# Optimization experiments

Measured on AMD Instinct MI355X. Metric: run time of the kernel, lower is better.

The kernel has to match this reference:

```python
import jax, jax.numpy as jnp
import numpy as np

EPS = 1e-06


def _create_circular_masks(h, w):
    # Faithful to the torch code: y spans width, x spans height -> mask shape (w, h).
    # Only used with square feature maps (h == w), matching the module's implicit assumption.
    cen_w, cen_h = w // 2, h // 2
    y = np.arange(-cen_w, w - cen_w).reshape(-1, 1)
    x = np.arange(-cen_h, h - cen_h).reshape(1, -1)
    y2, x2 = y * y, x * x
    r2 = x2 + y2
    masks = [r2 <= 0]
    max_r = int(np.sqrt(r2.max())) + 1
    quadrants = [(1, 1), (-1, 1), (1, -1), (-1, -1)]  # (sign_x, sign_y)
    for radius in range(1, max_r):
        lo, hi = (radius - 1) ** 2, radius ** 2
        for sx, sy in quadrants:
            quad = (sx * x >= 0) & (sy * y >= 0)
            masks.append((r2 > lo) & (r2 <= hi) & quad)  # ring mask
            masks.append((r2 <= hi) & quad)              # circle mask
    return np.stack(masks).astype(np.float32)  # [M, w, h] == [M, h, w] for square maps


def _l2_normalize(v):
    # v: [B, C]; torch norms over dim=1 with eps added to the norm
    return v / (jnp.linalg.norm(v, axis=1, keepdims=True) + EPS)


def setup_inputs() -> dict:
    key = jax.random.key(0)
    x = jax.random.normal(key, (32, 1024, 28, 28), dtype=jnp.float32)
    return {"x": x}


def reference(x) -> jnp.ndarray:
    B, C, H, W = x.shape
    masks = jnp.asarray(_create_circular_masks(H, W))  # [M, H, W] static constant
    # Global descriptor: max-pool over full map, then channel-wise L2 normalize.
    v = _l2_normalize(jnp.max(x, axis=(2, 3)))  # [B, C]
    # Accumulate masked-max descriptors; scan over the (fixed) mask set keeps
    # peak memory at one masked feature map instead of M of them.
    def step(acc, mask):
        vt = jnp.max(x * mask, axis=(2, 3))  # masked max-pool (zeros included, as in torch)
        return acc + _l2_normalize(vt), None
    v, _ = jax.lax.scan(step, v, masks)
    return v[:, :, None, None]  # [B, C, 1, 1] to match F.max_pool2d output shape
```

## Files before the change

kernel.cpp:

```cpp
#include <hip/hip_runtime.h>
#include <math.h>

#define B_DIM 32
#define C_DIM 1024
#define HW 28
#define MAP (HW * HW)
#define NMASK 153
#define NTERM 154
#define NBIN 77
#define DUMMY_BIN 77
#define MAXS 28

struct Sched {
    unsigned short tab[MAXS][64];
    unsigned char  split[64];
    unsigned char  binA[64];
    unsigned char  binB[64];
    bool ok;
};

constexpr Sched build_sched() {
    Sched S{};
    short px[NBIN][40] = {};
    int   n[NBIN] = {};
    for (int i = 0; i < 28; ++i)
        for (int j = 0; j < 28; ++j) {
            int dy = i - 14, dx = j - 14, r2 = dx * dx + dy * dy;
            int p = i * 28 + j;
            if (r2 == 0) { px[0][n[0]++] = (short)p; continue; }
            if (r2 > 361) continue;
            int r = 0; while (r * r < r2) ++r;
            const int sx[4] = {1, -1, 1, -1}, sy[4] = {1, 1, -1, -1};
            for (int q = 0; q < 4; ++q)
                if (sx[q] * dx >= 0 && sy[q] * dy >= 0) {
                    int b = 1 + q * 19 + (r - 1);
                    px[b][n[b]++] = (short)p;
                }
        }
    int ord[NBIN] = {};
    for (int k = 0; k < NBIN; ++k) ord[k] = k;
    for (int a = 0; a < NBIN; ++a) {
        int best = a;
        for (int b2 = a + 1; b2 < NBIN; ++b2)
            if (n[ord[b2]] > n[ord[best]]) best = b2;
        int t = ord[a]; ord[a] = ord[best]; ord[best] = t;
    }
    S.ok = true;
    for (int k = 0; k < NBIN; ++k) if (n[k] < 1 || n[k] > 40) S.ok = false;
    for (int l = 0; l < 64; ++l) {
        int bA = ord[l];
        int bB = (l >= 51) ? ord[64 + (63 - l)] : -1;
        int s = 0;
        for (int t = 0; t < n[bA] && s < MAXS; ++t) S.tab[s++][l] = (unsigned short)px[bA][t];
        S.split[l] = (unsigned char)s;
        S.binA[l]  = (unsigned char)bA;
        int fillpix;
        if (bB >= 0) {
            for (int t = 0; t < n[bB]; ++t) {
                if (s >= MAXS) { S.ok = false; break; }
                S.tab[s++][l] = (unsigned short)px[bB][t];
            }
            S.binB[l] = (unsigned char)bB;
            fillpix = px[bB][0];
        } else {
            S.binB[l] = DUMMY_BIN;
            fillpix = 406;
        }
        if (n[bA] > MAXS) S.ok = false;
        for (; s < MAXS; ++s) S.tab[s][l] = (unsigned short)fillpix;
    }
    return S;
}

static_assert(build_sched().ok, "schedule overflow / empty bin");
__constant__ Sched d_sched = build_sched();

__global__ __launch_bounds__(256) void cac_stage1(const float* __restrict__ x,
                                                  float* __restrict__ vt) {
    __shared__ __align__(16) float smap[4][MAP];
    __shared__ float sbin[4][NBIN + 1];
    __shared__ float spref[4][4][20];

    const int wave = threadIdx.x >> 6;
    const int lane = threadIdx.x & 63;
    const int pair = blockIdx.x * 4 + wave;

    const float4* xp4 = (const float4*)(x + (size_t)pair * MAP);
    float4* sm4 = (float4*)smap[wave];
    float gmax = -INFINITY;
    #pragma unroll
    for (int it = 0; it < 3; ++it) {
        float4 v = xp4[it * 64 + lane];
        sm4[it * 64 + lane] = v;
        gmax = fmaxf(fmaxf(gmax, fmaxf(v.x, v.y)), fmaxf(v.z, v.w));
    }
    if (lane < 4) {
        float4 v = xp4[192 + lane];
        sm4[192 + lane] = v;
        gmax = fmaxf(fmaxf(gmax, fmaxf(v.x, v.y)), fmaxf(v.z, v.w));
    }
    __syncthreads();

    const int split = d_sched.split[lane];
    float m1 = 0.0f, m2 = 0.0f;
    #pragma unroll
    for (int s = 0; s < MAXS; ++s) {
        float v = smap[wave][d_sched.tab[s][lane]];
        if (s < split) m1 = fmaxf(m1, v);
        else           m2 = fmaxf(m2, v);
    }
    sbin[wave][d_sched.binA[lane]] = m1;
    sbin[wave][d_sched.binB[lane]] = m2;

    #pragma unroll
    for (int off = 32; off; off >>= 1)
        gmax = fmaxf(gmax, __shfl_xor(gmax, off, 64));
    __syncthreads();

    if (lane < 4) {
        float run = sbin[wave][0];
        #pragma unroll
        for (int r = 1; r < 20; ++r) {
            run = fmaxf(run, sbin[wave][1 + lane * 19 + (r - 1)]);
            spref[wave][lane][r] = run;
        }
    }
    __syncthreads();

    const int b = pair >> 10;
    const int c = pair & (C_DIM - 1);
    float* outp = vt + (size_t)b * NTERM * C_DIM + c;
    for (int k = lane; k < NTERM; k += 64) {
        float val;
        if (k == 0) {
            val = sbin[wave][0];
        } else if (k == NMASK) {
            val = gmax;
        } else {
            int t = k - 1;
            int r = (t >> 3) + 1;
            int q = (t >> 1) & 3;
            val = (t & 1) ? spref[wave][q][r]
                          : sbin[wave][1 + q * 19 + (r - 1)];
        }
        outp[(size_t)k * C_DIM] = val;
    }
}

__global__ __launch_bounds__(256) void cac_stage2(const float* __restrict__ vt,
                                                  float* __restrict__ invn) {
    const int bm = blockIdx.x;
    const float4* p = (const float4*)(vt + (size_t)bm * C_DIM);
    float4 v = p[threadIdx.x];
    float s = v.x * v.x + v.y * v.y + v.z * v.z + v.w * v.w;
    __shared__ float red[4];
    #pragma unroll
    for (int off = 32; off; off >>= 1) s += __shfl_xor(s, off, 64);
    if ((threadIdx.x & 63) == 0) red[threadIdx.x >> 6] = s;
    __syncthreads();
    if (threadIdx.x == 0) {
        float t = red[0] + red[1] + red[2] + red[3];
        invn[bm] = 1.0f / (sqrtf(t) + 1e-6f);
    }
}

__global__ __launch_bounds__(256) void cac_stage3(const float* __restrict__ vt,
                                                  const float* __restrict__ invn,
                                                  float* __restrict__ out) {
    const int tid = blockIdx.x * 256 + threadIdx.x;
    const int b = tid >> 10;
    const int c = tid & (C_DIM - 1);
    const float* p  = vt + (size_t)b * NTERM * C_DIM + c;
    const float* nv = invn + b * NTERM;
    float acc0 = 0.0f, acc1 = 0.0f;
    #pragma unroll 7
    for (int m = 0; m < 154; m += 2) {
        acc0 += p[(size_t)m * C_DIM] * nv[m];
        acc1 += p[(size_t)(m + 1) * C_DIM] * nv[m + 1];
    }
    out[tid] = acc0 + acc1;
}

extern "C" void kernel_launch(void* const* d_in, const int* in_sizes, int n_in,
                              void* d_out, int out_size, void* d_ws, size_t ws_size,
                              hipStream_t stream) {
    const float* x = (const float*)d_in[0];
    float* out = (float*)d_out;

    float* vt   = (float*)d_ws;
    float* invn = vt + (size_t)B_DIM * NTERM * C_DIM;

    cac_stage1<<<(B_DIM * C_DIM) / 4, 256, 0, stream>>>(x, vt);
    cac_stage2<<<B_DIM * NTERM, 256, 0, stream>>>(vt, invn);
    cac_stage3<<<(B_DIM * C_DIM) / 256, 256, 0, stream>>>(vt, invn, out);
}
```

Baseline: 177.0 us.

## Store descriptors per pair contiguously, fuse norm partials, bank-balance LDS gathers

Stage 1 now writes each (b,c) pair's 160-term row contiguously instead of a strided [B,M,C] layout. It also emits per-block partial sums of squares, so stage 2 only reduces 256 partials per term rather than rereading the whole descriptor tensor. The gather schedule is split into separate 28-slot and 6-slot loops with byte offsets chosen at compile time to spread LDS bank load, which removes the per-iteration split branch. Stage 3 does float4 dot products over contiguous rows against shared inverse norms. In exchange the workspace grows with padding and a partials buffer, and stage B has only 32 blocks.

New measurement: 167.7 us. 5.3% less time.

```diff
diff --git a/kernel.cpp b/kernel.cpp
--- a/kernel.cpp
+++ b/kernel.cpp
@@ -4,16 +4,18 @@
 #define B_DIM 32
 #define C_DIM 1024
 #define HW 28
-#define MAP (HW * HW)
+#define MAP 784
 #define NMASK 153
 #define NTERM 154
+#define NROW 160
 #define NBIN 77
 #define DUMMY_BIN 77
-#define MAXS 28
+#define MAX1 28
+#define MAX2 6
 
 struct Sched {
-    unsigned short tab[MAXS][64];
-    unsigned char  split[64];
+    unsigned short off1[MAX1][64];
+    unsigned short off2[MAX2][64];
     unsigned char  binA[64];
     unsigned char  binB[64];
     bool ok;
@@ -21,6 +23,7 @@
 
 constexpr Sched build_sched() {
     Sched S{};
+    S.ok = true;
     short px[NBIN][40] = {};
     int   n[NBIN] = {};
     for (int i = 0; i < 28; ++i)
@@ -34,6 +37,7 @@
             for (int q = 0; q < 4; ++q)
                 if (sx[q] * dx >= 0 && sy[q] * dy >= 0) {
                     int b = 1 + q * 19 + (r - 1);
+                    if (n[b] >= 40) { S.ok = false; continue; }
                     px[b][n[b]++] = (short)p;
                 }
         }
@@ -41,45 +45,89 @@
     for (int k = 0; k < NBIN; ++k) ord[k] = k;
     for (int a = 0; a < NBIN; ++a) {
         int best = a;
-        for (int b2 = a + 1; b2 < NBIN; ++b2)
-            if (n[ord[b2]] > n[ord[best]]) best = b2;
+        for (int c = a + 1; c < NBIN; ++c)
+            if (n[ord[c]] > n[ord[best]]) best = c;
         int t = ord[a]; ord[a] = ord[best]; ord[best] = t;
     }
-    S.ok = true;
-    for (int k = 0; k < NBIN; ++k) if (n[k] < 1 || n[k] > 40) S.ok = false;
     for (int l = 0; l < 64; ++l) {
-        int bA = ord[l];
-        int bB = (l >= 51) ? ord[64 + (63 - l)] : -1;
-        int s = 0;
-        for (int t = 0; t < n[bA] && s < MAXS; ++t) S.tab[s++][l] = (unsigned short)px[bA][t];
-        S.split[l] = (unsigned char)s;
-        S.binA[l]  = (unsigned char)bA;
-        int fillpix;
-        if (bB >= 0) {
-            for (int t = 0; t < n[bB]; ++t) {
-                if (s >= MAXS) { S.ok = false; break; }
-                S.tab[s++][l] = (unsigned short)px[bB][t];
+        S.binA[l] = (unsigned char)ord[l];
+        S.binB[l] = (l >= 51) ? (unsigned char)ord[64 + (l - 51)]
+                              : (unsigned char)DUMMY_BIN;
+        if (n[ord[l]] > MAX1) S.ok = false;
+        if (l >= 51 && n[ord[64 + (l - 51)]] > MAX2) S.ok = false;
+    }
+    {
+        bool used[64][40] = {};
+        for (int s = 0; s < MAX1; ++s) {
+            int bankcnt[32] = {};
+            for (int l = 0; l < 64; ++l) {
+                int bin = S.binA[l], cnt = n[bin];
+                int bestp = 0, bestload = 1 << 30; bool haveUnused = false;
+                for (int t = 0; t < cnt; ++t)
+                    if (!used[l][t]) {
+                        int load = bankcnt[px[bin][t] % 32];
+                        if (!haveUnused || load < bestload) { haveUnused = true; bestload = load; bestp = t; }
+                    }
+                if (!haveUnused)
+                    for (int t = 0; t < cnt; ++t) {
+                        int load = bankcnt[px[bin][t] % 32];
+                        if (load < bestload) { bestload = load; bestp = t; }
+                    }
+                int p = px[bin][bestp];
+                if (haveUnused) used[l][bestp] = true;
+                S.off1[s][l] = (unsigned short)(p * 4);
+                bankcnt[p % 32]++;
             }
-            S.binB[l] = (unsigned char)bB;
-            fillpix = px[bB][0];
-        } else {
-            S.binB[l] = DUMMY_BIN;
-            fillpix = 406;
-        }
-        if (n[bA] > MAXS) S.ok = false;
-        for (; s < MAXS; ++s) S.tab[s][l] = (unsigned short)fillpix;
+        }
+        for (int l = 0; l < 64; ++l)
+            for (int t = 0; t < n[S.binA[l]]; ++t)
+                if (!used[l][t]) S.ok = false;
+    }
+    {
+        bool used[64][40] = {};
+        for (int s = 0; s < MAX2; ++s) {
+            int bankcnt[32] = {};
+            for (int l = 0; l < 64; ++l) {
+                if (S.binB[l] == DUMMY_BIN) {
+                    S.off2[s][l] = (unsigned short)((l % 32) * 4);
+                    continue;
+                }
+                int bin = S.binB[l], cnt = n[bin];
+                int bestp = 0, bestload = 1 << 30; bool haveUnused = false;
+                for (int t = 0; t < cnt; ++t)
+                    if (!used[l][t]) {
+                        int load = bankcnt[px[bin][t] % 32];
+                        if (!haveUnused || load < bestload) { haveUnused = true; bestload = load; bestp = t; }
+                    }
+                if (!haveUnused)
+                    for (int t = 0; t < cnt; ++t) {
+                        int load = bankcnt[px[bin][t] % 32];
+                        if (load < bestload) { bestload = load; bestp = t; }
+                    }
+                int p = px[bin][bestp];
+                if (haveUnused) used[l][bestp] = true;
+                S.off2[s][l] = (unsigned short)(p * 4);
+                bankcnt[p % 32]++;
+            }
+        }
+        for (int l = 0; l < 64; ++l)
+            if (S.binB[l] != DUMMY_BIN)
+                for (int t = 0; t < n[S.binB[l]]; ++t)
+                    if (!used[l][t]) S.ok = false;
     }
     return S;
 }
 
-static_assert(build_sched().ok, "schedule overflow / empty bin");
+static_assert(build_sched().ok, "schedule overflow / unplaced pixel");
 __constant__ Sched d_sched = build_sched();
 
-__global__ __launch_bounds__(256) void cac_stage1(const float* __restrict__ x,
-                                                  float* __restrict__ vt) {
+__global__ __launch_bounds__(256) void cac_stageA(const float* __restrict__ x,
+                                                  float* __restrict__ vt,
+                                                  float* __restrict__ partial) {
     __shared__ __align__(16) float smap[4][MAP];
     __shared__ float sbin[4][NBIN + 1];
     __shared__ float spref[4][4][20];
+    __shared__ float ssq[4][NROW];
 
     const int wave = threadIdx.x >> 6;
     const int lane = threadIdx.x & 63;
@@ -101,14 +149,15 @@
     }
     __syncthreads();
 
-    const int split = d_sched.split[lane];
+    const char* base = (const char*)smap[wave];
     float m1 = 0.0f, m2 = 0.0f;
     #pragma unroll
-    for (int s = 0; s < MAXS; ++s) {
-        float v = smap[wave][d_sched.tab[s][lane]];
-        if (s < split) m1 = fmaxf(m1, v);
-        else           m2 = fmaxf(m2, v);
-    }
+    for (int s = 0; s < MAX1; ++s)
+        m1 = fmaxf(m1, *(const float*)(base + d_sched.off1[s][lane]));
+    #pragma unroll
+    for (int s = 0; s < MAX2; ++s)
+        m2 = fmaxf(m2, *(const float*)(base + d_sched.off2[s][lane]));
+
     sbin[wave][d_sched.binA[lane]] = m1;
     sbin[wave][d_sched.binB[lane]] = m2;
 
@@ -127,58 +176,61 @@
     }
     __syncthreads();
 
-    const int b = pair >> 10;
-    const int c = pair & (C_DIM - 1);
-    float* outp = vt + (size_t)b * NTERM * C_DIM + c;
-    for (int k = lane; k < NTERM; k += 64) {
-        float val;
-        if (k == 0) {
-            val = sbin[wave][0];
-        } else if (k == NMASK) {
-            val = gmax;
-        } else {
-            int t = k - 1;
-            int r = (t >> 3) + 1;
-            int q = (t >> 1) & 3;
-            val = (t & 1) ? spref[wave][q][r]
-                          : sbin[wave][1 + q * 19 + (r - 1)];
-        }
-        outp[(size_t)k * C_DIM] = val;
-    }
-}
-
-__global__ __launch_bounds__(256) void cac_stage2(const float* __restrict__ vt,
+    float* rowp = vt + (size_t)pair * NROW;
+    #pragma unroll
+    for (int i = 0; i < 3; ++i) {
+        int k = lane + i * 64;
+        if (k < NROW) {
+            float val;
+            if (k == 0) val = sbin[wave][0];
+            else if (k == NMASK) val = gmax;
+            else if (k < NMASK) {
+                int t = k - 1, r = (t >> 3) + 1, q = (t >> 1) & 3;
+                val = (t & 1) ? spref[wave][q][r]
+                              : sbin[wave][1 + q * 19 + (r - 1)];
+            } else val = 0.0f;
+            rowp[k] = val;
+            ssq[wave][k] = val * val;
+        }
+    }
+    __syncthreads();
+
+    if (threadIdx.x < NROW) {
+        int t = threadIdx.x;
+        partial[(size_t)blockIdx.x * NROW + t] =
+            ssq[0][t] + ssq[1][t] + ssq[2][t] + ssq[3][t];
+    }
+}
+
+__global__ __launch_bounds__(192) void cac_stageB(const float* __restrict__ partial,
                                                   float* __restrict__ invn) {
-    const int bm = blockIdx.x;
-    const float4* p = (const float4*)(vt + (size_t)bm * C_DIM);
-    float4 v = p[threadIdx.x];
-    float s = v.x * v.x + v.y * v.y + v.z * v.z + v.w * v.w;
-    __shared__ float red[4];
-    #pragma unroll
-    for (int off = 32; off; off >>= 1) s += __shfl_xor(s, off, 64);
-    if ((threadIdx.x & 63) == 0) red[threadIdx.x >> 6] = s;
-    __syncthreads();
-    if (threadIdx.x == 0) {
-        float t = red[0] + red[1] + red[2] + red[3];
-        invn[bm] = 1.0f / (sqrtf(t) + 1e-6f);
-    }
-}
-
-__global__ __launch_bounds__(256) void cac_stage3(const float* __restrict__ vt,
+    const int b = blockIdx.x, t = threadIdx.x;
+    if (t >= NROW) return;
+    const float* p = partial + (size_t)b * 256 * NROW + t;
+    float s = 0.0f;
+    #pragma unroll 8
+    for (int r = 0; r < 256; ++r) s += p[(size_t)r * NROW];
+    invn[b * NROW + t] = (t < NTERM) ? 1.0f / (sqrtf(s) + 1e-6f) : 0.0f;
+}
+
+__global__ __launch_bounds__(128) void cac_stageC(const float* __restrict__ vt,
                                                   const float* __restrict__ invn,
                                                   float* __restrict__ out) {
-    const int tid = blockIdx.x * 256 + threadIdx.x;
-    const int b = tid >> 10;
-    const int c = tid & (C_DIM - 1);
-    const float* p  = vt + (size_t)b * NTERM * C_DIM + c;
-    const float* nv = invn + b * NTERM;
-    float acc0 = 0.0f, acc1 = 0.0f;
-    #pragma unroll 7
-    for (int m = 0; m < 154; m += 2) {
-        acc0 += p[(size_t)m * C_DIM] * nv[m];
-        acc1 += p[(size_t)(m + 1) * C_DIM] * nv[m + 1];
-    }
-    out[tid] = acc0 + acc1;
+    __shared__ __align__(16) float sinv[NROW];
+    const int pair = blockIdx.x * 128 + threadIdx.x;
+    const int b = pair >> 10;
+    for (int i = threadIdx.x; i < NROW; i += 128)
+        sinv[i] = invn[b * NROW + i];
+    __syncthreads();
+    const float4* row = (const float4*)(vt + (size_t)pair * NROW);
+    const float4* w4 = (const float4*)sinv;
+    float acc = 0.0f;
+    #pragma unroll
+    for (int i = 0; i < NROW / 4; ++i) {
+        float4 v = row[i], w = w4[i];
+        acc += v.x * w.x + v.y * w.y + v.z * w.z + v.w * w.w;
+    }
+    out[pair] = acc;
 }
 
 extern "C" void kernel_launch(void* const* d_in, const int* in_sizes, int n_in,
@@ -187,10 +239,11 @@
     const float* x = (const float*)d_in[0];
     float* out = (float*)d_out;
 
-    float* vt   = (float*)d_ws;
-    float* invn = vt + (size_t)B_DIM * NTERM * C_DIM;
-
-    cac_stage1<<<(B_DIM * C_DIM) / 4, 256, 0, stream>>>(x, vt);
-    cac_stage2<<<B_DIM * NTERM, 256, 0, stream>>>(vt, invn);
-    cac_stage3<<<(B_DIM * C_DIM) / 256, 256, 0, stream>>>(vt, invn, out);
-}
+    float* vt      = (float*)d_ws;
+    float* partial = vt + (size_t)B_DIM * C_DIM * NROW;
+    float* invn    = partial + (size_t)8192 * NROW;
+
+    cac_stageA<<<(B_DIM * C_DIM) / 4, 256, 0, stream>>>(x, vt, partial);
+    cac_stageB<<<B_DIM, 192, 0, stream>>>(partial, invn);
+    cac_stageC<<<(B_DIM * C_DIM) / 128, 128, 0, stream>>>(vt, invn, out);
+}
```
